# Kernel optimization log

Measured on AMD Instinct MI355X. Metric: run time of the kernel, lower is better.

Reference implementation:

```python
import jax, jax.numpy as jnp
import numpy as np

# Hardcoded 6-node part graph from the module (src, dst) pairs; PyG flows src->dst.
_EDGES = np.array([[0,1],[0,2],[0,3],[0,4],[0,5],[1,2],[1,3],[1,4],[1,5],[2,3],[2,4],[3,5],[4,5],[1,0],[2,0],[3,0],[4,0],[5,0],[2,1],[3,1],[4,1],[5,1],[3,2],[4,2],[5,3],[5,4]], dtype=np.int32)
SRC = jnp.asarray(_EDGES[:, 0])
DST = jnp.asarray(_EDGES[:, 1])
NUM_NODES = 6


def setup_inputs() -> dict:
    key = jax.random.key(0)
    k0, k1, k2 = jax.random.split(key, 3)
    C, B = 128, 32768
    x = jax.random.normal(k0, (NUM_NODES, B, C), dtype=jnp.float32)
    # SAGEConv weights: lin_l (aggregated neighbors, carries bias) and lin_r (root)
    W_l = jax.random.normal(k1, (2 * C, C), dtype=jnp.float32) / np.sqrt(C).astype(np.float32)
    W_r = jax.random.normal(k2, (2 * C, C), dtype=jnp.float32) / np.sqrt(C).astype(np.float32)
    b = jnp.zeros((2 * C,), dtype=jnp.float32)
    return {"x": x, "W_l": W_l, "W_r": W_r, "b": b}


def reference(x, W_l, W_r, b):
    # x: [N=6, B, C]
    # mean aggregation of source features at each destination node
    msg = x[SRC]                                                  # [E, B, C]
    agg = jax.ops.segment_sum(msg, DST, num_segments=NUM_NODES)   # [N, B, C]
    deg = jax.ops.segment_sum(jnp.ones_like(DST, dtype=x.dtype), DST, num_segments=NUM_NODES)
    agg = agg / deg[:, None, None]
    # SAGEConv: lin_l(agg) + lin_r(x), bias in lin_l
    y = jnp.einsum('nbc,oc->nbo', agg, W_l) + b + jnp.einsum('nbc,oc->nbo', x, W_r)
    y = jax.nn.gelu(y, approximate=False)                         # torch F.gelu = exact erf
    # Python cat-loop over nodes == concatenate the 6 node slices along features
    N, B, O = y.shape
    return jnp.transpose(y, (1, 0, 2)).reshape(B, N * O)          # [B, 6*2C]
```

## Files before the change

### kernel.cpp

```cpp
#include <hip/hip_runtime.h>
#include <hip/hip_bf16.h>

#define NB 32768
#define CD 128
#define NNODES 6
#define OUTW 1536
#define KW 256

typedef __attribute__((ext_vector_type(8))) short short8;
typedef __attribute__((ext_vector_type(4))) short s16x4;
typedef __attribute__((ext_vector_type(4))) float f32x4;

static __device__ __forceinline__ short f2bf(float f) {
    union { __bf16 b; short s; } u;
    u.b = (__bf16)f;
    return u.s;
}

static __device__ __forceinline__ short8 pack8(f32x4 a, f32x4 b) {
    short8 p;
    #pragma unroll
    for (int j = 0; j < 4; ++j) { p[j] = f2bf(a[j]); p[4 + j] = f2bf(b[j]); }
    return p;
}

static __device__ __forceinline__ s16x4 pack4(f32x4 a) {
    s16x4 p;
    #pragma unroll
    for (int j = 0; j < 4; ++j) p[j] = f2bf(a[j]);
    return p;
}

__global__ void prep_w(const float* __restrict__ Wl, const float* __restrict__ Wr,
                       short* __restrict__ Wb) {
    const int i = (blockIdx.x * 256 + threadIdx.x) * 8;
    const int o = i >> 8;
    const int k = i & 255;
    const float* src = (k < 128) ? (Wl + o * CD + k) : (Wr + o * CD + (k - 128));
    *(short8*)(Wb + i) = pack8(*(const f32x4*)src, *(const f32x4*)(src + 4));
}

#define LIDX(p, r, k) ((((p) << 11) + ((r) << 7) + (k)) ^ (((r) & 7) << 3))

__global__ __launch_bounds__(512, 2)
void sage_v8(const float* __restrict__ x, const short* __restrict__ Wb,
             const float* __restrict__ bias, float* __restrict__ out) {
    __shared__ __align__(16) short A[10 * 16 * 128];

    const int t = threadIdx.x;
    const size_t row0 = (size_t)blockIdx.x * 16;

    {
        const int r = t >> 5;
        const int c = t & 31;
        const float* pb = x + (row0 + r) * CD + c * 4;
        f32x4 v0 = *(const f32x4*)(pb + 0ull * (NB * CD));
        f32x4 v1 = *(const f32x4*)(pb + 1ull * (NB * CD));
        f32x4 v2 = *(const f32x4*)(pb + 2ull * (NB * CD));
        f32x4 v3 = *(const f32x4*)(pb + 3ull * (NB * CD));
        f32x4 v4 = *(const f32x4*)(pb + 4ull * (NB * CD));
        f32x4 v5 = *(const f32x4*)(pb + 5ull * (NB * CD));
        f32x4 S01 = v0 + v1, S25 = v2 + v5, S34 = v3 + v4;
        f32x4 T = S01 + S25 + S34;
        const int k = c * 4;
        *(s16x4*)&A[LIDX(0, r, k)] = pack4((T - v0) * 0.2f);
        *(s16x4*)&A[LIDX(1, r, k)] = pack4((T - v1) * 0.2f);
        *(s16x4*)&A[LIDX(2, r, k)] = pack4((S01 + S34) * 0.25f);
        *(s16x4*)&A[LIDX(3, r, k)] = pack4((S01 + S25) * 0.25f);
        *(s16x4*)&A[LIDX(4, r, k)] = pack4(v0);
        *(s16x4*)&A[LIDX(5, r, k)] = pack4(v1);
        *(s16x4*)&A[LIDX(6, r, k)] = pack4(v2);
        *(s16x4*)&A[LIDX(7, r, k)] = pack4(v3);
        *(s16x4*)&A[LIDX(8, r, k)] = pack4(v4);
        *(s16x4*)&A[LIDX(9, r, k)] = pack4(v5);
    }
    __syncthreads();

    const int lane = t & 63;
    const int wv = t >> 6;
    const int lo = lane & 15;
    const int hi = lane >> 4;
    const int obase = wv * 32;

    f32x4 acc[NNODES][2];
    #pragma unroll
    for (int n = 0; n < NNODES; ++n)
        #pragma unroll
        for (int i = 0; i < 2; ++i) acc[n][i] = (f32x4){0.f, 0.f, 0.f, 0.f};

    #pragma unroll
    for (int m = 0; m < 4; ++m) {
        const int kk = m * 32 + hi * 8;
        short8 fg0  = *(const short8*)&A[LIDX(0, lo, kk)];
        short8 fg1  = *(const short8*)&A[LIDX(1, lo, kk)];
        short8 fg25 = *(const short8*)&A[LIDX(2, lo, kk)];
        short8 fg34 = *(const short8*)&A[LIDX(3, lo, kk)];
        short8 fx0 = *(const short8*)&A[LIDX(4, lo, kk)];
        short8 fx1 = *(const short8*)&A[LIDX(5, lo, kk)];
        short8 fx2 = *(const short8*)&A[LIDX(6, lo, kk)];
        short8 fx3 = *(const short8*)&A[LIDX(7, lo, kk)];
        short8 fx4 = *(const short8*)&A[LIDX(8, lo, kk)];
        short8 fx5 = *(const short8*)&A[LIDX(9, lo, kk)];

        #pragma unroll
        for (int i = 0; i < 2; ++i) {
            const int o = obase + i * 16 + lo;
            short8 wa = *(const short8*)&Wb[o * KW + kk];
            short8 wx = *(const short8*)&Wb[o * KW + 128 + kk];
            acc[0][i] = __builtin_amdgcn_mfma_f32_16x16x32_bf16(wa, fg0,  acc[0][i], 0, 0, 0);
            acc[1][i] = __builtin_amdgcn_mfma_f32_16x16x32_bf16(wa, fg1,  acc[1][i], 0, 0, 0);
            acc[2][i] = __builtin_amdgcn_mfma_f32_16x16x32_bf16(wa, fg25, acc[2][i], 0, 0, 0);
            acc[3][i] = __builtin_amdgcn_mfma_f32_16x16x32_bf16(wa, fg34, acc[3][i], 0, 0, 0);
            acc[4][i] = __builtin_amdgcn_mfma_f32_16x16x32_bf16(wa, fg34, acc[4][i], 0, 0, 0);
            acc[5][i] = __builtin_amdgcn_mfma_f32_16x16x32_bf16(wa, fg25, acc[5][i], 0, 0, 0);
            acc[0][i] = __builtin_amdgcn_mfma_f32_16x16x32_bf16(wx, fx0, acc[0][i], 0, 0, 0);
            acc[1][i] = __builtin_amdgcn_mfma_f32_16x16x32_bf16(wx, fx1, acc[1][i], 0, 0, 0);
            acc[2][i] = __builtin_amdgcn_mfma_f32_16x16x32_bf16(wx, fx2, acc[2][i], 0, 0, 0);
            acc[3][i] = __builtin_amdgcn_mfma_f32_16x16x32_bf16(wx, fx3, acc[3][i], 0, 0, 0);
            acc[4][i] = __builtin_amdgcn_mfma_f32_16x16x32_bf16(wx, fx4, acc[4][i], 0, 0, 0);
            acc[5][i] = __builtin_amdgcn_mfma_f32_16x16x32_bf16(wx, fx5, acc[5][i], 0, 0, 0);
        }
    }

    #pragma unroll
    for (int n = 0; n < NNODES; ++n) {
        #pragma unroll
        for (int i = 0; i < 2; ++i) {
            const int ocol = obase + i * 16 + hi * 4;
            f32x4 v = acc[n][i] + *(const f32x4*)&bias[ocol];
            f32x4 g;
            #pragma unroll
            for (int j = 0; j < 4; ++j) {
                const float s = v[j] * (0.7978845608f + 0.0356774081f * v[j] * v[j]);
                const float r = __builtin_amdgcn_exp2f(-2.885390082f * s);
                g[j] = v[j] * __builtin_amdgcn_rcpf(1.0f + r);
            }
            *(f32x4*)&out[(row0 + lo) * OUTW + n * 256 + ocol] = g;
        }
    }
}

extern "C" void kernel_launch(void* const* d_in, const int* in_sizes, int n_in,
                              void* d_out, int out_size, void* d_ws, size_t ws_size,
                              hipStream_t stream) {
    const float* x  = (const float*)d_in[0];
    const float* Wl = (const float*)d_in[1];
    const float* Wr = (const float*)d_in[2];
    const float* b  = (const float*)d_in[3];
    float* out = (float*)d_out;
    short* Wb = (short*)d_ws;

    prep_w<<<dim3(32), dim3(256), 0, stream>>>(Wl, Wr, Wb);
    sage_v8<<<dim3(NB / 16), dim3(512), 0, stream>>>(x, Wb, b, out);
}
```

Measured before the change: 101.6 us.

## Make blocks persistent over 8 row groups with double-buffered async LDS loads

Each block now processes eight 16-row groups instead of one, and uses global_load_lds to prefetch the next group's x tiles into a double-buffered fp32 LDS staging area while the current group's MFMAs and GELU epilogue run. The aim is to hide global load latency behind compute and to amortise launch and weight-fetch overhead across groups. In exchange it adds 96KB of LDS per block, which likely cuts occupancy below the two blocks per CU the launch bounds request, and it leaves only 256 blocks. It also adds extra barriers per iteration.

```diff
diff --git a/kernel.cpp b/kernel.cpp
--- a/kernel.cpp
+++ b/kernel.cpp
@@ -6,6 +6,8 @@
 #define NNODES 6
 #define OUTW 1536
 #define KW 256
+#define GPB 8
+#define NBLK (NB / 16 / GPB)
 
 typedef __attribute__((ext_vector_type(8))) short short8;
 typedef __attribute__((ext_vector_type(4))) short s16x4;
@@ -43,23 +45,41 @@
 #define LIDX(p, r, k) ((((p) << 11) + ((r) << 7) + (k)) ^ (((r) & 7) << 3))
 
 __global__ __launch_bounds__(512, 2)
-void sage_v8(const float* __restrict__ x, const short* __restrict__ Wb,
+void sage_v9(const float* __restrict__ x, const short* __restrict__ Wb,
              const float* __restrict__ bias, float* __restrict__ out) {
+    __shared__ __align__(16) float raw[2][NNODES * 16 * 128];
     __shared__ __align__(16) short A[10 * 16 * 128];
 
     const int t = threadIdx.x;
-    const size_t row0 = (size_t)blockIdx.x * 16;
+    const int r = t >> 5;
+    const int c = t & 31;
+    const int lane = t & 63;
+    const int wv = t >> 6;
+    const int lo = lane & 15;
+    const int hi = lane >> 4;
+    const int obase = wv * 32;
+    const size_t rg0 = (size_t)blockIdx.x * GPB;
 
-    {
-        const int r = t >> 5;
-        const int c = t & 31;
-        const float* pb = x + (row0 + r) * CD + c * 4;
-        f32x4 v0 = *(const f32x4*)(pb + 0ull * (NB * CD));
-        f32x4 v1 = *(const f32x4*)(pb + 1ull * (NB * CD));
-        f32x4 v2 = *(const f32x4*)(pb + 2ull * (NB * CD));
-        f32x4 v3 = *(const f32x4*)(pb + 3ull * (NB * CD));
-        f32x4 v4 = *(const f32x4*)(pb + 4ull * (NB * CD));
-        f32x4 v5 = *(const f32x4*)(pb + 5ull * (NB * CD));
+    auto stage = [&](int buf, size_t rg) {
+        const float* gp = x + (rg * 16 + r) * CD + c * 4;
+        #pragma unroll
+        for (int s = 0; s < NNODES; ++s) {
+            __builtin_amdgcn_global_load_lds(
+                (const __attribute__((address_space(1))) void*)(gp + (size_t)s * (NB * CD)),
+                (__attribute__((address_space(3))) void*)&raw[buf][s * 2048 + wv * 256],
+                16, 0, 0);
+        }
+    };
+
+    auto convert = [&](int buf) {
+        const float* rb = &raw[buf][0];
+        const int base = r * 128 + c * 4;
+        f32x4 v0 = *(const f32x4*)&rb[0 * 2048 + base];
+        f32x4 v1 = *(const f32x4*)&rb[1 * 2048 + base];
+        f32x4 v2 = *(const f32x4*)&rb[2 * 2048 + base];
+        f32x4 v3 = *(const f32x4*)&rb[3 * 2048 + base];
+        f32x4 v4 = *(const f32x4*)&rb[4 * 2048 + base];
+        f32x4 v5 = *(const f32x4*)&rb[5 * 2048 + base];
         f32x4 S01 = v0 + v1, S25 = v2 + v5, S34 = v3 + v4;
         f32x4 T = S01 + S25 + S34;
         const int k = c * 4;
@@ -73,69 +93,78 @@
         *(s16x4*)&A[LIDX(7, r, k)] = pack4(v3);
         *(s16x4*)&A[LIDX(8, r, k)] = pack4(v4);
         *(s16x4*)&A[LIDX(9, r, k)] = pack4(v5);
-    }
+    };
+
+    stage(0, rg0);
+    __syncthreads();
+    convert(0);
     __syncthreads();
 
-    const int lane = t & 63;
-    const int wv = t >> 6;
-    const int lo = lane & 15;
-    const int hi = lane >> 4;
-    const int obase = wv * 32;
+    #pragma unroll 1
+    for (int it = 0; it < GPB; ++it) {
+        if (it + 1 < GPB) stage((it + 1) & 1, rg0 + it + 1);
 
-    f32x4 acc[NNODES][2];
-    #pragma unroll
-    for (int n = 0; n < NNODES; ++n)
+        f32x4 acc[NNODES][2];
         #pragma unroll
-        for (int i = 0; i < 2; ++i) acc[n][i] = (f32x4){0.f, 0.f, 0.f, 0.f};
-
-    #pragma unroll
-    for (int m = 0; m < 4; ++m) {
-        const int kk = m * 32 + hi * 8;
-        short8 fg0  = *(const short8*)&A[LIDX(0, lo, kk)];
-        short8 fg1  = *(const short8*)&A[LIDX(1, lo, kk)];
-        short8 fg25 = *(const short8*)&A[LIDX(2, lo, kk)];
-        short8 fg34 = *(const short8*)&A[LIDX(3, lo, kk)];
-        short8 fx0 = *(const short8*)&A[LIDX(4, lo, kk)];
-        short8 fx1 = *(const short8*)&A[LIDX(5, lo, kk)];
-        short8 fx2 = *(const short8*)&A[LIDX(6, lo, kk)];
-        short8 fx3 = *(const short8*)&A[LIDX(7, lo, kk)];
-        short8 fx4 = *(const short8*)&A[LIDX(8, lo, kk)];
-        short8 fx5 = *(const short8*)&A[LIDX(9, lo, kk)];
+        for (int n = 0; n < NNODES; ++n)
+            #pragma unroll
+            for (int i = 0; i < 2; ++i) acc[n][i] = (f32x4){0.f, 0.f, 0.f, 0.f};
 
         #pragma unroll
-        for (int i = 0; i < 2; ++i) {
-            const int o = obase + i * 16 + lo;
-            short8 wa = *(const short8*)&Wb[o * KW + kk];
-            short8 wx = *(const short8*)&Wb[o * KW + 128 + kk];
-            acc[0][i] = __builtin_amdgcn_mfma_f32_16x16x32_bf16(wa, fg0,  acc[0][i], 0, 0, 0);
-            acc[1][i] = __builtin_amdgcn_mfma_f32_16x16x32_bf16(wa, fg1,  acc[1][i], 0, 0, 0);
-            acc[2][i] = __builtin_amdgcn_mfma_f32_16x16x32_bf16(wa, fg25, acc[2][i], 0, 0, 0);
-            acc[3][i] = __builtin_amdgcn_mfma_f32_16x16x32_bf16(wa, fg34, acc[3][i], 0, 0, 0);
-            acc[4][i] = __builtin_amdgcn_mfma_f32_16x16x32_bf16(wa, fg34, acc[4][i], 0, 0, 0);
-            acc[5][i] = __builtin_amdgcn_mfma_f32_16x16x32_bf16(wa, fg25, acc[5][i], 0, 0, 0);
-            acc[0][i] = __builtin_amdgcn_mfma_f32_16x16x32_bf16(wx, fx0, acc[0][i], 0, 0, 0);
-            acc[1][i] = __builtin_amdgcn_mfma_f32_16x16x32_bf16(wx, fx1, acc[1][i], 0, 0, 0);
-            acc[2][i] = __builtin_amdgcn_mfma_f32_16x16x32_bf16(wx, fx2, acc[2][i], 0, 0, 0);
-            acc[3][i] = __builtin_amdgcn_mfma_f32_16x16x32_bf16(wx, fx3, acc[3][i], 0, 0, 0);
-            acc[4][i] = __builtin_amdgcn_mfma_f32_16x16x32_bf16(wx, fx4, acc[4][i], 0, 0, 0);
-            acc[5][i] = __builtin_amdgcn_mfma_f32_16x16x32_bf16(wx, fx5, acc[5][i], 0, 0, 0);
+        for (int m = 0; m < 4; ++m) {
+            const int kk = m * 32 + hi * 8;
+            short8 fg0  = *(const short8*)&A[LIDX(0, lo, kk)];
+            short8 fg1  = *(const short8*)&A[LIDX(1, lo, kk)];
+            short8 fg25 = *(const short8*)&A[LIDX(2, lo, kk)];
+            short8 fg34 = *(const short8*)&A[LIDX(3, lo, kk)];
+            short8 fx0 = *(const short8*)&A[LIDX(4, lo, kk)];
+            short8 fx1 = *(const short8*)&A[LIDX(5, lo, kk)];
+            short8 fx2 = *(const short8*)&A[LIDX(6, lo, kk)];
+            short8 fx3 = *(const short8*)&A[LIDX(7, lo, kk)];
+            short8 fx4 = *(const short8*)&A[LIDX(8, lo, kk)];
+            short8 fx5 = *(const short8*)&A[LIDX(9, lo, kk)];
+            #pragma unroll
+            for (int i = 0; i < 2; ++i) {
+                const int o = obase + i * 16 + lo;
+                short8 wa = *(const short8*)&Wb[o * KW + kk];
+                short8 wx = *(const short8*)&Wb[o * KW + 128 + kk];
+                acc[0][i] = __builtin_amdgcn_mfma_f32_16x16x32_bf16(wa, fg0,  acc[0][i], 0, 0, 0);
+                acc[1][i] = __builtin_amdgcn_mfma_f32_16x16x32_bf16(wa, fg1,  acc[1][i], 0, 0, 0);
+                acc[2][i] = __builtin_amdgcn_mfma_f32_16x16x32_bf16(wa, fg25, acc[2][i], 0, 0, 0);
+                acc[3][i] = __builtin_amdgcn_mfma_f32_16x16x32_bf16(wa, fg34, acc[3][i], 0, 0, 0);
+                acc[4][i] = __builtin_amdgcn_mfma_f32_16x16x32_bf16(wa, fg34, acc[4][i], 0, 0, 0);
+                acc[5][i] = __builtin_amdgcn_mfma_f32_16x16x32_bf16(wa, fg25, acc[5][i], 0, 0, 0);
+                acc[0][i] = __builtin_amdgcn_mfma_f32_16x16x32_bf16(wx, fx0, acc[0][i], 0, 0, 0);
+                acc[1][i] = __builtin_amdgcn_mfma_f32_16x16x32_bf16(wx, fx1, acc[1][i], 0, 0, 0);
+                acc[2][i] = __builtin_amdgcn_mfma_f32_16x16x32_bf16(wx, fx2, acc[2][i], 0, 0, 0);
+                acc[3][i] = __builtin_amdgcn_mfma_f32_16x16x32_bf16(wx, fx3, acc[3][i], 0, 0, 0);
+                acc[4][i] = __builtin_amdgcn_mfma_f32_16x16x32_bf16(wx, fx4, acc[4][i], 0, 0, 0);
+                acc[5][i] = __builtin_amdgcn_mfma_f32_16x16x32_bf16(wx, fx5, acc[5][i], 0, 0, 0);
+            }
         }
-    }
 
-    #pragma unroll
-    for (int n = 0; n < NNODES; ++n) {
+        const size_t orow = (rg0 + it) * 16 + lo;
         #pragma unroll
-        for (int i = 0; i < 2; ++i) {
-            const int ocol = obase + i * 16 + hi * 4;
-            f32x4 v = acc[n][i] + *(const f32x4*)&bias[ocol];
-            f32x4 g;
+        for (int n = 0; n < NNODES; ++n) {
             #pragma unroll
-            for (int j = 0; j < 4; ++j) {
-                const float s = v[j] * (0.7978845608f + 0.0356774081f * v[j] * v[j]);
-                const float r = __builtin_amdgcn_exp2f(-2.885390082f * s);
-                g[j] = v[j] * __builtin_amdgcn_rcpf(1.0f + r);
+            for (int i = 0; i < 2; ++i) {
+                const int ocol = obase + i * 16 + hi * 4;
+                f32x4 v = acc[n][i] + *(const f32x4*)&bias[ocol];
+                f32x4 g;
+                #pragma unroll
+                for (int j = 0; j < 4; ++j) {
+                    const float s = v[j] * (0.7978845608f + 0.0356774081f * v[j] * v[j]);
+                    const float rr = __builtin_amdgcn_exp2f(-2.885390082f * s);
+                    g[j] = v[j] * __builtin_amdgcn_rcpf(1.0f + rr);
+                }
+                *(f32x4*)&out[orow * OUTW + n * 256 + ocol] = g;
             }
-            *(f32x4*)&out[(row0 + lo) * OUTW + n * 256 + ocol] = g;
+        }
+
+        __syncthreads();
+        if (it + 1 < GPB) {
+            convert((it + 1) & 1);
+            __syncthreads();
         }
     }
 }
@@ -151,5 +180,5 @@
     short* Wb = (short*)d_ws;
 
     prep_w<<<dim3(32), dim3(256), 0, stream>>>(Wl, Wr, Wb);
-    sage_v8<<<dim3(NB / 16), dim3(512), 0, stream>>>(x, Wb, b, out);
+    sage_v9<<<dim3(NBLK), dim3(512), 0, stream>>>(x, Wb, b, out);
 }
```

Result: faster. 92.21 us (-9.2%).
